# Optimization experiments

Hardware: AMD Instinct MI355X
Metric: run time of the kernel (lower is better)

The kernel has to match this reference:

```python
import jax, jax.numpy as jnp
import numpy as np

H = 128
M = 50000
L = 400000
EPS = 1e-9


def setup_inputs() -> dict:
    key = jax.random.key(0)
    ks = jax.random.split(key, 24)
    d = {
        'x_emb': jax.random.normal(ks[0], (M, H), jnp.float32),
        'child_h': jax.random.normal(ks[1], (M, H), jnp.float32),
        'child_c': jax.random.normal(ks[2], (M, H), jnp.float32),
        'pair_cand_idx': jax.random.randint(ks[3], (L,), 0, M, jnp.int32),
        'pair_child_idx': jax.random.randint(ks[4], (L,), 0, M, jnp.int32),
    }
    s = 1.0 / np.sqrt(H)
    names = ['Wi_w', 'Ui_w', 'Wf_w', 'Uf_w', 'Wo_w', 'Uo_w', 'Wc_w', 'Uc_w', 'Wa_w', 'Ua_w']
    for i, n in enumerate(names):
        d[n] = jax.random.uniform(ks[5 + i], (H, H), jnp.float32, -s, s)
    for i, n in enumerate(['Wi_b', 'Wf_b', 'Wo_b', 'Wc_b', 'Wa_b']):
        d[n] = jax.random.uniform(ks[15 + i], (H,), jnp.float32, -s, s)
    d['v_w'] = jax.random.uniform(ks[20], (H,), jnp.float32, -s, s)
    return d


def reference(x_emb, child_h, child_c, pair_cand_idx, pair_child_idx,
              Wi_w, Ui_w, Wf_w, Uf_w, Wo_w, Uo_w, Wc_w, Uc_w, Wa_w, Ua_w,
              Wi_b, Wf_b, Wo_b, Wc_b, Wa_b, v_w):
    m = x_emb.shape[0]
    ci, chi = pair_cand_idx, pair_child_idx

    # --- segment attention (torch version runs under no_grad) ---
    Ah = child_h @ Wa_w.T + Wa_b          # [M,H]
    Bx = x_emb @ Ua_w.T                   # [M,H]
    e = jnp.tanh(Ah[chi] + Bx[ci]) @ v_w  # [L]
    seg_max = jax.ops.segment_max(e, ci, num_segments=m)
    x_exp = jnp.exp(e - seg_max[ci])
    seg_sum = jax.ops.segment_sum(x_exp, ci, num_segments=m) + EPS
    attn = x_exp / seg_sum[ci]            # [L]
    h_hat = jax.ops.segment_sum(attn[:, None] * child_h[chi], ci, num_segments=m)  # [M,H]

    # --- tree-LSTM gates ---
    i_j = jax.nn.sigmoid(x_emb @ Wi_w.T + Wi_b + h_hat @ Ui_w.T)
    Wfx = x_emb @ Wf_w.T + Wf_b
    Ufh = child_h @ Uf_w.T
    f_pair = jax.nn.sigmoid(Wfx[ci] + Ufh[chi])                       # [L,H]
    sum_f_c = jax.ops.segment_sum(f_pair * child_c[chi], ci, num_segments=m)
    c_t = jnp.tanh(x_emb @ Wc_w.T + Wc_b + h_hat @ Uc_w.T)
    c = i_j * c_t + sum_f_c
    o_j = jax.nn.sigmoid(x_emb @ Wo_w.T + Wo_b + h_hat @ Uo_w.T)
    h = o_j * jnp.tanh(c)
    return (h, c)
```

## Files before the change

### kernel.cpp

```cpp
#include <hip/hip_runtime.h>
#include <cstdint>
#include <cstddef>

#define H 128
#define PSTRIDE 512

typedef __bf16 v8bf __attribute__((ext_vector_type(8)));
typedef __bf16 v4bf __attribute__((ext_vector_type(4)));
typedef float  v4f  __attribute__((ext_vector_type(4)));

__device__ __forceinline__ float ftanh(float x) {
    return 1.f - 2.f / (1.f + __expf(2.f * x));
}
__device__ __forceinline__ float fsigm(float x) {
    return 1.f / (1.f + __expf(-x));
}

__device__ __forceinline__ float red32(float s) {
    int x;
    x = __builtin_amdgcn_update_dpp(0, __float_as_int(s), 0xB1, 0xF, 0xF, true);
    s += __int_as_float(x);
    x = __builtin_amdgcn_update_dpp(0, __float_as_int(s), 0x4E, 0xF, 0xF, true);
    s += __int_as_float(x);
    x = __builtin_amdgcn_update_dpp(0, __float_as_int(s), 0x141, 0xF, 0xF, true);
    s += __int_as_float(x);
    x = __builtin_amdgcn_update_dpp(0, __float_as_int(s), 0x140, 0xF, 0xF, true);
    s += __int_as_float(x);
    x = __builtin_amdgcn_ds_swizzle(__float_as_int(s), 0x401F);
    return s + __int_as_float(x);
}

struct MatDesc {
    const __bf16* A;
    int           lda;
    const __bf16* Wb;
    const float*  bias;
    __bf16*       C;
    int           ldc;
};
struct MatBatch { MatDesc m[5]; };
struct WPtrs { const float* w[10]; };

__global__ __launch_bounds__(256) void prep_k(WPtrs wp, __bf16* __restrict__ Wb,
                                              const float* __restrict__ x,
                                              __bf16* __restrict__ xe,
                                              const int* __restrict__ ci,
                                              int* __restrict__ counts,
                                              int MH4, int L) {
    int tid = blockIdx.x * 256 + threadIdx.x;
    if (tid < 40960) {
        int mat = tid >> 12;
        int off = (tid & 4095) << 2;
        v4f a = *(const v4f*)(wp.w[mat] + off);
        v4bf b;
#pragma unroll
        for (int k = 0; k < 4; ++k) b[k] = (__bf16)a[k];
        *(v4bf*)(Wb + mat * 16384 + off) = b;
        return;
    }
    int i = tid - 40960;
    if (i < MH4) {
        v4f a = ((const v4f*)x)[i];
        v4bf ab;
#pragma unroll
        for (int k = 0; k < 4; ++k) ab[k] = (__bf16)a[k];
        ((v4bf*)xe)[i] = ab;
        return;
    }
    int l = i - MH4;
    if (l < L) atomicAdd(&counts[ci[l]], 1);
}

__global__ __launch_bounds__(256) void pair_k(const float* __restrict__ chh,
                                              const float* __restrict__ chc,
                                              const __bf16* __restrict__ Wa,
                                              const __bf16* __restrict__ Uf,
                                              const float* __restrict__ bia,
                                              __bf16* __restrict__ P,
                                              int M, int ntile) {
    const int blk = blockIdx.x;
    const int w16 = blk % 16;
    const int t   = (blk / 16) * 8 + (w16 & 7);
    const int nh  = w16 >> 3;
    if (t >= ntile) return;

    __shared__ __bf16 lds[2][64][136];

    for (int tt = threadIdx.x; tt < 2048; tt += 256) {
        int ws = tt >> 10;
        int ln = (tt >> 4) & 63;
        int k  = (tt & 15) << 3;
        const __bf16* src = ws ? Uf : Wa;
        *(v8bf*)&lds[ws][ln][k] = *(const v8bf*)(src + (nh * 64 + ln) * H + k);
    }
    __syncthreads();

    const int wave = threadIdx.x >> 6;
    const int lane = threadIdx.x & 63;
    const int quad = lane >> 4;
    const int l16  = lane & 15;
    const int r0   = t * 128 + wave * 32;

    int ra = r0 + l16;      if (ra > M - 1) ra = M - 1;
    int rb = r0 + 16 + l16; if (rb > M - 1) rb = M - 1;

    const float* p0 = chh + (size_t)ra * H + quad * 8;
    const float* p1 = chh + (size_t)rb * H + quad * 8;
    v8bf a0[4], a1[4];
#pragma unroll
    for (int k0 = 0; k0 < 4; ++k0) {
        v4f x0a = *(const v4f*)(p0 + k0 * 32);
        v4f x0b = *(const v4f*)(p0 + k0 * 32 + 4);
        v4f x1a = *(const v4f*)(p1 + k0 * 32);
        v4f x1b = *(const v4f*)(p1 + k0 * 32 + 4);
        v8bf t0, t1;
#pragma unroll
        for (int k = 0; k < 4; ++k) {
            t0[k] = (__bf16)x0a[k]; t0[k + 4] = (__bf16)x0b[k];
            t1[k] = (__bf16)x1a[k]; t1[k + 4] = (__bf16)x1b[k];
        }
        a0[k0] = t0; a1[k0] = t1;
    }

    v4f acc[2][4][2];
#pragma unroll
    for (int ws = 0; ws < 2; ++ws)
#pragma unroll
        for (int ntl = 0; ntl < 4; ++ntl)
#pragma unroll
            for (int rg = 0; rg < 2; ++rg) acc[ws][ntl][rg] = (v4f){0.f, 0.f, 0.f, 0.f};

#pragma unroll
    for (int k0 = 0; k0 < 4; ++k0) {
#pragma unroll
        for (int ntl = 0; ntl < 4; ++ntl) {
            v8bf bwa = *(const v8bf*)(&lds[0][ntl * 16 + l16][k0 * 32 + quad * 8]);
            v8bf buf = *(const v8bf*)(&lds[1][ntl * 16 + l16][k0 * 32 + quad * 8]);
            acc[0][ntl][0] = __builtin_amdgcn_mfma_f32_16x16x32_bf16(a0[k0], bwa, acc[0][ntl][0], 0, 0, 0);
            acc[0][ntl][1] = __builtin_amdgcn_mfma_f32_16x16x32_bf16(a1[k0], bwa, acc[0][ntl][1], 0, 0, 0);
            acc[1][ntl][0] = __builtin_amdgcn_mfma_f32_16x16x32_bf16(a0[k0], buf, acc[1][ntl][0], 0, 0, 0);
            acc[1][ntl][1] = __builtin_amdgcn_mfma_f32_16x16x32_bf16(a1[k0], buf, acc[1][ntl][1], 0, 0, 0);
        }
    }
    __syncthreads();

    __bf16 (*stg)[128][68] = reinterpret_cast<__bf16 (*)[128][68]>(&lds[0][0][0]);
#pragma unroll
    for (int ws = 0; ws < 2; ++ws)
#pragma unroll
        for (int ntl = 0; ntl < 4; ++ntl) {
            int lcol = ntl * 16 + l16;
            float bv = (ws == 0) ? bia[nh * 64 + lcol] : 0.f;
#pragma unroll
            for (int rg = 0; rg < 2; ++rg)
#pragma unroll
                for (int r = 0; r < 4; ++r) {
                    int lrow = wave * 32 + rg * 16 + quad * 4 + r;
                    stg[ws][lrow][lcol] = (__bf16)(acc[ws][ntl][rg][r] + bv);
                }
        }
    __syncthreads();

    for (int id = threadIdx.x; id < 2048; id += 256) {
        int lrow = id >> 4;
        int lq   = id & 15;
        int m = t * 128 + lrow;
        if (m >= M) continue;
        int q = nh * 16 + lq;
        v4f hv = *(const v4f*)(chh + (size_t)m * H + q * 4);
        v4f cv = *(const v4f*)(chc + (size_t)m * H + q * 4);
        v8bf o0, o1;
#pragma unroll
        for (int kk = 0; kk < 4; ++kk) {
            o0[kk]     = (__bf16)hv[kk];
            o0[4 + kk] = (__bf16)cv[kk];
            o1[kk]     = stg[1][lrow][lq * 4 + kk];
            o1[4 + kk] = stg[0][lrow][lq * 4 + kk];
        }
        __bf16* dst = P + (size_t)m * PSTRIDE + ((size_t)q << 4);
        *(v8bf*)dst = o0;
        *(v8bf*)(dst + 8) = o1;
    }
}

__global__ __launch_bounds__(256) void gemm_batch(MatBatch batch, int M, int ntile) {
    const int blk = blockIdx.x;
    const int g = blk / 40;
    const int w = blk % 40;
    const int j = w >> 3;
    const int t = (g << 3) | (w & 7);
    if (t >= ntile) return;
    const MatDesc d = batch.m[j];
    __shared__ __bf16 wlds[H][H + 8];

    for (int tt = threadIdx.x; tt < 2048; tt += 256) {
        int n = tt >> 4;
        int k = (tt & 15) << 3;
        *(v8bf*)&wlds[n][k] = *(const v8bf*)(d.Wb + n * H + k);
    }
    __syncthreads();

    const int wave = threadIdx.x >> 6;
    const int lane = threadIdx.x & 63;
    const int quad = lane >> 4;
    const int l16  = lane & 15;
    const int r0   = t * 128 + wave * 32;

    int ra = r0 + l16;      if (ra > M - 1) ra = M - 1;
    int rb = r0 + 16 + l16; if (rb > M - 1) rb = M - 1;

    const __bf16* p0 = d.A + (size_t)ra * d.lda + quad * 8;
    const __bf16* p1 = d.A + (size_t)rb * d.lda + quad * 8;
    v8bf a0[4], a1[4];
#pragma unroll
    for (int k0 = 0; k0 < 4; ++k0) {
        a0[k0] = *(const v8bf*)(p0 + k0 * 32);
        a1[k0] = *(const v8bf*)(p1 + k0 * 32);
    }

    v4f acc0[8], acc1[8];
#pragma unroll
    for (int nt = 0; nt < 8; ++nt) {
        acc0[nt] = (v4f){0.f, 0.f, 0.f, 0.f};
        acc1[nt] = (v4f){0.f, 0.f, 0.f, 0.f};
    }

#pragma unroll
    for (int k0 = 0; k0 < 4; ++k0) {
#pragma unroll
        for (int nt = 0; nt < 8; ++nt) {
            v8bf b = *(const v8bf*)(&wlds[nt * 16 + l16][k0 * 32 + quad * 8]);
            acc0[nt] = __builtin_amdgcn_mfma_f32_16x16x32_bf16(a0[k0], b, acc0[nt], 0, 0, 0);
            acc1[nt] = __builtin_amdgcn_mfma_f32_16x16x32_bf16(a1[k0], b, acc1[nt], 0, 0, 0);
        }
    }

#pragma unroll
    for (int nt = 0; nt < 8; ++nt) {
        int n = nt * 16 + l16;
        float bia = d.bias ? d.bias[n] : 0.f;
#pragma unroll
        for (int r = 0; r < 4; ++r) {
            int m0 = r0 + quad * 4 + r;
            int m1 = m0 + 16;
            if (m0 < M) d.C[(size_t)m0 * d.ldc + n] = (__bf16)(acc0[nt][r] + bia);
            if (m1 < M) d.C[(size_t)m1 * d.ldc + n] = (__bf16)(acc1[nt][r] + bia);
        }
    }
}

__global__ __launch_bounds__(1024) void scan_local(const int* __restrict__ counts,
                                                   int* __restrict__ excl,
                                                   int* __restrict__ bsums, int M) {
    __shared__ int s[1024];
    int tid = threadIdx.x;
    int idx = blockIdx.x * 1024 + tid;
    int v = (idx < M) ? counts[idx] : 0;
    s[tid] = v;
    __syncthreads();
    for (int off = 1; off < 1024; off <<= 1) {
        int t = (tid >= off) ? s[tid - off] : 0;
        __syncthreads();
        s[tid] += t;
        __syncthreads();
    }
    if (idx < M) excl[idx] = s[tid] - v;
    if (tid == 1023) bsums[blockIdx.x] = s[1023];
}

__global__ __launch_bounds__(1024) void scan_fused(int* __restrict__ rowptr,
                                                   int* __restrict__ cursor,
                                                   const int* __restrict__ bsums,
                                                   const int* __restrict__ counts,
                                                   int M, int nb) {
    __shared__ int s[1024];
    int t = threadIdx.x, b = blockIdx.x;
    int v = (t < nb) ? bsums[t] : 0;
    s[t] = v;
    __syncthreads();
    for (int off = 1; off < 1024; off <<= 1) {
        int tt = (t >= off) ? s[t - off] : 0;
        __syncthreads();
        s[t] += tt;
        __syncthreads();
    }
    int boff = (b == 0) ? 0 : s[b - 1];
    int idx = b * 1024 + t;
    if (idx < M) {
        int val = rowptr[idx] + boff;
        rowptr[idx] = val;
        cursor[idx] = val;
        if (idx == M - 1) rowptr[M] = val + counts[M - 1];
    }
}

__global__ __launch_bounds__(256) void scatter_k(const int* __restrict__ ci,
                                                 const int* __restrict__ chi,
                                                 int* __restrict__ cursor,
                                                 int* __restrict__ payload, int L) {
    int l = blockIdx.x * 256 + threadIdx.x;
    if (l < L) {
        int pos = atomicAdd(&cursor[ci[l]], 1);
        payload[pos] = chi[l];
    }
}

__global__ __launch_bounds__(128) void segment_fused(const int* __restrict__ rowptr,
                                                     const int* __restrict__ payload,
                                                     const float* __restrict__ vw,
                                                     const __bf16* __restrict__ Bx,
                                                     const __bf16* __restrict__ Wfx,
                                                     const __bf16* __restrict__ P,
                                                     __bf16* __restrict__ hhat,
                                                     float* __restrict__ sumfc, int M) {
    const int wl   = threadIdx.x & 63;
    const int half = wl & 32;
    const int l32  = wl & 31;
    const int m = blockIdx.x * 4 + (threadIdx.x >> 5);
    if (m >= M) return;
    const int start = rowptr[m];
    const int deg   = rowptr[m + 1] - start;
    const int h   = l32 << 2;
    const int q16 = l32 << 4;

    v4bf bx4 = *(const v4bf*)(Bx + (m << 7) + h);
    v4bf wf4 = *(const v4bf*)(Wfx + (m << 7) + h);
    v4f  vv  = *(const v4f*)(vw + h);
    float bxf[4], wff[4];
#pragma unroll
    for (int k = 0; k < 4; ++k) { bxf[k] = (float)bx4[k]; wff[k] = (float)wf4[k]; }

    int pl0 = (l32 < deg) ? payload[start + l32] : 0;
    int pl1 = (32 + l32 < deg) ? payload[start + 32 + l32] : 0;

    float denom = 0.f;
    float acch[4] = {0.f, 0.f, 0.f, 0.f};
    float accf[4] = {0.f, 0.f, 0.f, 0.f};

    const int jcap = deg < 64 ? deg : 64;
    if (jcap > 0) {
        int cj0 = __shfl(pl0, half, 64);
        const __bf16* pb0 = P + ((size_t)cj0 << 9) + q16;
        v8bf x0 = *(const v8bf*)pb0;
        v8bf x1 = *(const v8bf*)(pb0 + 8);
        for (int j = 0; j < jcap; ++j) {
            v8bf y0 = x0, y1 = x1;
            int jn = j + 1;
            if (jn < jcap) {
                int cjn = __shfl((jn & 32) ? pl1 : pl0, half | (jn & 31), 64);
                const __bf16* pbn = P + ((size_t)cjn << 9) + q16;
                x0 = *(const v8bf*)pbn;
                x1 = *(const v8bf*)(pbn + 8);
            }
            float s = 0.f;
#pragma unroll
            for (int k = 0; k < 4; ++k) s += ftanh((float)y1[4 + k] + bxf[k]) * vv[k];
            s = red32(s);
            float ex = __expf(s);
            denom += ex;
#pragma unroll
            for (int k = 0; k < 4; ++k) {
                acch[k] = fmaf(ex, (float)y0[k], acch[k]);
                accf[k] += fsigm(wff[k] + (float)y1[k]) * (float)y0[4 + k];
            }
        }
    }
    for (int j = 64; j < deg; ++j) {
        int cj = payload[start + j];
        const __bf16* pb = P + ((size_t)cj << 9) + q16;
        v8bf x0 = *(const v8bf*)pb;
        v8bf x1 = *(const v8bf*)(pb + 8);
        float s = 0.f;
#pragma unroll
        for (int k = 0; k < 4; ++k) s += ftanh((float)x1[4 + k] + bxf[k]) * vv[k];
        s = red32(s);
        float ex = __expf(s);
        denom += ex;
#pragma unroll
        for (int k = 0; k < 4; ++k) {
            acch[k] = fmaf(ex, (float)x0[k], acch[k]);
            accf[k] += fsigm(wff[k] + (float)x1[k]) * (float)x0[4 + k];
        }
    }

    float inv = 1.f / (denom + 1e-9f);
    v4bf hb;
    v4f sf;
#pragma unroll
    for (int k = 0; k < 4; ++k) { hb[k] = (__bf16)(acch[k] * inv); sf[k] = accf[k]; }
    *(v4bf*)(hhat + (size_t)m * H + h) = hb;
    *(v4f*)(sumfc + (size_t)m * H + h) = sf;
}

__global__ __launch_bounds__(256) void gemm_final(const __bf16* __restrict__ hhat,
                                                  const __bf16* __restrict__ Ui,
                                                  const __bf16* __restrict__ Uc,
                                                  const __bf16* __restrict__ Uo,
                                                  const __bf16* __restrict__ Xi,
                                                  const __bf16* __restrict__ Xc,
                                                  const __bf16* __restrict__ Xo,
                                                  const float* __restrict__ sumfc,
                                                  float* __restrict__ out, int M, int MH) {
    const int wave = threadIdx.x >> 6;
    const int lane = threadIdx.x & 63;
    const int quad = lane >> 4;
    const int l16  = lane & 15;
    const int r0   = blockIdx.x * 128 + wave * 32;
    const int nt0  = blockIdx.y * 2;

    const __bf16* p0 = hhat + (size_t)(r0 + l16) * H + quad * 8;
    const __bf16* p1 = hhat + (size_t)(r0 + 16 + l16) * H + quad * 8;
    v8bf a0[4], a1[4];
#pragma unroll
    for (int k0 = 0; k0 < 4; ++k0) {
        a0[k0] = *(const v8bf*)(p0 + k0 * 32);
        a1[k0] = *(const v8bf*)(p1 + k0 * 32);
    }

#pragma unroll
    for (int ntl = 0; ntl < 2; ++ntl) {
        const int nt = nt0 + ntl;
        const int boff = (nt * 16 + l16) * H + quad * 8;
        v4f ai0 = (v4f){0.f, 0.f, 0.f, 0.f}, ai1 = ai0;
        v4f ac0 = ai0, ac1 = ai0, ao0 = ai0, ao1 = ai0;
#pragma unroll
        for (int k0 = 0; k0 < 4; ++k0) {
            v8bf bi = *(const v8bf*)(Ui + boff + k0 * 32);
            v8bf bc = *(const v8bf*)(Uc + boff + k0 * 32);
            v8bf bo = *(const v8bf*)(Uo + boff + k0 * 32);
            ai0 = __builtin_amdgcn_mfma_f32_16x16x32_bf16(a0[k0], bi, ai0, 0, 0, 0);
            ai1 = __builtin_amdgcn_mfma_f32_16x16x32_bf16(a1[k0], bi, ai1, 0, 0, 0);
            ac0 = __builtin_amdgcn_mfma_f32_16x16x32_bf16(a0[k0], bc, ac0, 0, 0, 0);
            ac1 = __builtin_amdgcn_mfma_f32_16x16x32_bf16(a1[k0], bc, ac1, 0, 0, 0);
            ao0 = __builtin_amdgcn_mfma_f32_16x16x32_bf16(a0[k0], bo, ao0, 0, 0, 0);
            ao1 = __builtin_amdgcn_mfma_f32_16x16x32_bf16(a1[k0], bo, ao1, 0, 0, 0);
        }
        int n = nt * 16 + l16;
#pragma unroll
        for (int r = 0; r < 4; ++r) {
            int m0 = r0 + quad * 4 + r;
            if (m0 < M) {
                size_t idx = (size_t)m0 * H + n;
                float ig = fsigm((float)Xi[idx] + ai0[r]);
                float ct = ftanh((float)Xc[idx] + ac0[r]);
                float og = fsigm((float)Xo[idx] + ao0[r]);
                float c = ig * ct + sumfc[idx];
                out[idx] = og * ftanh(c);
                out[MH + idx] = c;
            }
            int m1 = m0 + 16;
            if (m1 < M) {
                size_t idx = (size_t)m1 * H + n;
                float ig = fsigm((float)Xi[idx] + ai1[r]);
                float ct = ftanh((float)Xc[idx] + ac1[r]);
                float og = fsigm((float)Xo[idx] + ao1[r]);
                float c = ig * ct + sumfc[idx];
                out[idx] = og * ftanh(c);
                out[MH + idx] = c;
            }
        }
    }
}

extern "C" void kernel_launch(void* const* d_in, const int* in_sizes, int n_in,
                              void* d_out, int out_size, void* d_ws, size_t ws_size,
                              hipStream_t stream) {
    const float* x_emb   = (const float*)d_in[0];
    const float* child_h = (const float*)d_in[1];
    const float* child_c = (const float*)d_in[2];
    const int*   ci      = (const int*)d_in[3];
    const int*   chi     = (const int*)d_in[4];
    const float* Wi_b = (const float*)d_in[15];
    const float* Wf_b = (const float*)d_in[16];
    const float* Wo_b = (const float*)d_in[17];
    const float* Wc_b = (const float*)d_in[18];
    const float* Wa_b = (const float*)d_in[19];
    const float* vw   = (const float*)d_in[20];

    const int M    = in_sizes[0] / H;
    const int L    = in_sizes[3];
    const int Mpad = (M + 127) & ~127;
    const int MH   = M * H;
    const int MH4  = MH / 4;

    char* p = (char*)d_ws;
    auto alloc = [&](size_t bytes) {
        char* r = p;
        p += (bytes + 255) & ~(size_t)255;
        return (void*)r;
    };
    size_t bfbytes = (size_t)Mpad * H * sizeof(__bf16);
    __bf16* xe16   = (__bf16*)alloc(bfbytes);
    __bf16* P      = (__bf16*)alloc((size_t)Mpad * PSTRIDE * sizeof(__bf16));
    __bf16* hhat16 = (__bf16*)alloc(bfbytes);
    __bf16* Bx16   = (__bf16*)alloc(bfbytes);
    __bf16* Wfx16  = (__bf16*)alloc(bfbytes);
    __bf16* Xi16   = (__bf16*)alloc(bfbytes);
    __bf16* Xc16   = (__bf16*)alloc(bfbytes);
    __bf16* Xo16   = (__bf16*)alloc(bfbytes);
    __bf16* Wb     = (__bf16*)alloc(10 * 16384 * sizeof(__bf16));
    float* sumfc   = (float*)alloc((size_t)MH * 4);
    int*   payload = (int*)alloc((size_t)L * 4);
    int*   counts  = (int*)alloc((size_t)M * 4);
    int*   rowptr  = (int*)alloc((size_t)(M + 1) * 4);
    int*   cursor  = (int*)alloc((size_t)M * 4);
    int*   bsums   = (int*)alloc(1024 * 4);

    hipMemsetAsync(counts, 0, (size_t)M * 4, stream);

    WPtrs wp;
    for (int k = 0; k < 10; ++k) wp.w[k] = (const float*)d_in[5 + k];
    int prep_items = 40960 + MH4 + L;
    prep_k<<<(prep_items + 255) / 256, 256, 0, stream>>>(wp, Wb, x_emb, xe16,
                                                         ci, counts, MH4, L);

    const __bf16* Wi = Wb + 0 * 16384;
    const __bf16* Ui = Wb + 1 * 16384;
    const __bf16* Wf = Wb + 2 * 16384;
    const __bf16* Uf = Wb + 3 * 16384;
    const __bf16* Wo = Wb + 4 * 16384;
    const __bf16* Uo = Wb + 5 * 16384;
    const __bf16* Wc = Wb + 6 * 16384;
    const __bf16* Uc = Wb + 7 * 16384;
    const __bf16* Wa = Wb + 8 * 16384;
    const __bf16* Ua = Wb + 9 * 16384;

    const int ntile = Mpad / 128;
    const int ntile8 = (ntile + 7) & ~7;

    pair_k<<<2 * ntile8, 256, 0, stream>>>(child_h, child_c, Wa, Uf, Wa_b, P, M, ntile);

    MatBatch ba{};
    ba.m[0] = MatDesc{xe16, H, Ua, nullptr, Bx16,  H};
    ba.m[1] = MatDesc{xe16, H, Wf, Wf_b,    Wfx16, H};
    ba.m[2] = MatDesc{xe16, H, Wi, Wi_b,    Xi16,  H};
    ba.m[3] = MatDesc{xe16, H, Wc, Wc_b,    Xc16,  H};
    ba.m[4] = MatDesc{xe16, H, Wo, Wo_b,    Xo16,  H};
    gemm_batch<<<5 * ntile8, 256, 0, stream>>>(ba, M, ntile);

    int nb = (M + 1023) / 1024;
    scan_local<<<nb, 1024, 0, stream>>>(counts, rowptr, bsums, M);
    scan_fused<<<nb, 1024, 0, stream>>>(rowptr, cursor, bsums, counts, M, nb);

    scatter_k<<<(L + 255) / 256, 256, 0, stream>>>(ci, chi, cursor, payload, L);

    segment_fused<<<(M + 3) / 4, 128, 0, stream>>>(rowptr, payload, vw, Bx16, Wfx16, P,
                                                   hhat16, sumfc, M);

    gemm_final<<<dim3(Mpad / 128, 4), 256, 0, stream>>>(hhat16, Ui, Uc, Uo, Xi16, Xc16, Xo16,
                                                        sumfc, (float*)d_out, M, MH);
}
```

Baseline: 416.1 us.

## Merge pair and batch GEMM kernels, convert weights to bf16 on load

Folds the child_h pair GEMM kernel and the five x_emb GEMMs into one launch of 7 block-groups per tile. The separate weight-conversion pass and its workspace buffer are dropped, and fp32 weights are now converted to bf16 when staged into LDS or loaded in gemm_final. This removes a kernel launch and a global round trip for the bf16 weights. In exchange every block, and every gemm_final iteration, repeats the fp32 conversion. The segment loop's software prefetch of the next P row is also removed, which may expose gather latency.

```diff
diff --git a/kernel.cpp b/kernel.cpp
--- a/kernel.cpp
+++ b/kernel.cpp
@@ -14,6 +14,15 @@
 }
 __device__ __forceinline__ float fsigm(float x) {
     return 1.f / (1.f + __expf(-x));
+}
+
+__device__ __forceinline__ v8bf cvt8(const float* p) {
+    v4f a = *(const v4f*)p;
+    v4f b = *(const v4f*)(p + 4);
+    v8bf r;
+#pragma unroll
+    for (int k = 0; k < 4; ++k) { r[k] = (__bf16)a[k]; r[4 + k] = (__bf16)b[k]; }
+    return r;
 }
 
 __device__ __forceinline__ float red32(float s) {
@@ -30,35 +39,24 @@
     return s + __int_as_float(x);
 }
 
-struct MatDesc {
-    const __bf16* A;
-    int           lda;
-    const __bf16* Wb;
-    const float*  bias;
-    __bf16*       C;
-    int           ldc;
+struct XMat { const float* W; const float* bias; __bf16* C; };
+struct GemmAll {
+    const __bf16* xe;
+    XMat xm[5];
+    const float* chh;
+    const float* chc;
+    const float* Wa;
+    const float* Uf;
+    const float* bia;
+    __bf16* P;
 };
-struct MatBatch { MatDesc m[5]; };
-struct WPtrs { const float* w[10]; };
-
-__global__ __launch_bounds__(256) void prep_k(WPtrs wp, __bf16* __restrict__ Wb,
-                                              const float* __restrict__ x,
+
+__global__ __launch_bounds__(256) void prep_k(const float* __restrict__ x,
                                               __bf16* __restrict__ xe,
                                               const int* __restrict__ ci,
                                               int* __restrict__ counts,
                                               int MH4, int L) {
-    int tid = blockIdx.x * 256 + threadIdx.x;
-    if (tid < 40960) {
-        int mat = tid >> 12;
-        int off = (tid & 4095) << 2;
-        v4f a = *(const v4f*)(wp.w[mat] + off);
-        v4bf b;
-#pragma unroll
-        for (int k = 0; k < 4; ++k) b[k] = (__bf16)a[k];
-        *(v4bf*)(Wb + mat * 16384 + off) = b;
-        return;
-    }
-    int i = tid - 40960;
+    int i = blockIdx.x * 256 + threadIdx.x;
     if (i < MH4) {
         v4f a = ((const v4f*)x)[i];
         v4bf ab;
@@ -71,29 +69,15 @@
     if (l < L) atomicAdd(&counts[ci[l]], 1);
 }
 
-__global__ __launch_bounds__(256) void pair_k(const float* __restrict__ chh,
-                                              const float* __restrict__ chc,
-                                              const __bf16* __restrict__ Wa,
-                                              const __bf16* __restrict__ Uf,
-                                              const float* __restrict__ bia,
-                                              __bf16* __restrict__ P,
-                                              int M, int ntile) {
+__global__ __launch_bounds__(256) void gemm_all(GemmAll ga, int M, int ntile) {
     const int blk = blockIdx.x;
-    const int w16 = blk % 16;
-    const int t   = (blk / 16) * 8 + (w16 & 7);
-    const int nh  = w16 >> 3;
+    const int g = blk / 56;
+    const int w = blk % 56;
+    const int j = w >> 3;
+    const int t = (g << 3) | (w & 7);
     if (t >= ntile) return;
 
-    __shared__ __bf16 lds[2][64][136];
-
-    for (int tt = threadIdx.x; tt < 2048; tt += 256) {
-        int ws = tt >> 10;
-        int ln = (tt >> 4) & 63;
-        int k  = (tt & 15) << 3;
-        const __bf16* src = ws ? Uf : Wa;
-        *(v8bf*)&lds[ws][ln][k] = *(const v8bf*)(src + (nh * 64 + ln) * H + k);
-    }
-    __syncthreads();
+    __shared__ __bf16 lds_raw[17408];
 
     const int wave = threadIdx.x >> 6;
     const int lane = threadIdx.x & 63;
@@ -104,147 +88,135 @@
     int ra = r0 + l16;      if (ra > M - 1) ra = M - 1;
     int rb = r0 + 16 + l16; if (rb > M - 1) rb = M - 1;
 
-    const float* p0 = chh + (size_t)ra * H + quad * 8;
-    const float* p1 = chh + (size_t)rb * H + quad * 8;
-    v8bf a0[4], a1[4];
-#pragma unroll
-    for (int k0 = 0; k0 < 4; ++k0) {
-        v4f x0a = *(const v4f*)(p0 + k0 * 32);
-        v4f x0b = *(const v4f*)(p0 + k0 * 32 + 4);
-        v4f x1a = *(const v4f*)(p1 + k0 * 32);
-        v4f x1b = *(const v4f*)(p1 + k0 * 32 + 4);
-        v8bf t0, t1;
-#pragma unroll
-        for (int k = 0; k < 4; ++k) {
-            t0[k] = (__bf16)x0a[k]; t0[k + 4] = (__bf16)x0b[k];
-            t1[k] = (__bf16)x1a[k]; t1[k + 4] = (__bf16)x1b[k];
-        }
-        a0[k0] = t0; a1[k0] = t1;
-    }
-
-    v4f acc[2][4][2];
-#pragma unroll
-    for (int ws = 0; ws < 2; ++ws)
-#pragma unroll
-        for (int ntl = 0; ntl < 4; ++ntl)
-#pragma unroll
-            for (int rg = 0; rg < 2; ++rg) acc[ws][ntl][rg] = (v4f){0.f, 0.f, 0.f, 0.f};
-
-#pragma unroll
-    for (int k0 = 0; k0 < 4; ++k0) {
-#pragma unroll
-        for (int ntl = 0; ntl < 4; ++ntl) {
-            v8bf bwa = *(const v8bf*)(&lds[0][ntl * 16 + l16][k0 * 32 + quad * 8]);
-            v8bf buf = *(const v8bf*)(&lds[1][ntl * 16 + l16][k0 * 32 + quad * 8]);
-            acc[0][ntl][0] = __builtin_amdgcn_mfma_f32_16x16x32_bf16(a0[k0], bwa, acc[0][ntl][0], 0, 0, 0);
-            acc[0][ntl][1] = __builtin_amdgcn_mfma_f32_16x16x32_bf16(a1[k0], bwa, acc[0][ntl][1], 0, 0, 0);
-            acc[1][ntl][0] = __builtin_amdgcn_mfma_f32_16x16x32_bf16(a0[k0], buf, acc[1][ntl][0], 0, 0, 0);
-            acc[1][ntl][1] = __builtin_amdgcn_mfma_f32_16x16x32_bf16(a1[k0], buf, acc[1][ntl][1], 0, 0, 0);
-        }
-    }
-    __syncthreads();
-
-    __bf16 (*stg)[128][68] = reinterpret_cast<__bf16 (*)[128][68]>(&lds[0][0][0]);
-#pragma unroll
-    for (int ws = 0; ws < 2; ++ws)
-#pragma unroll
-        for (int ntl = 0; ntl < 4; ++ntl) {
-            int lcol = ntl * 16 + l16;
-            float bv = (ws == 0) ? bia[nh * 64 + lcol] : 0.f;
-#pragma unroll
-            for (int rg = 0; rg < 2; ++rg)
-#pragma unroll
-                for (int r = 0; r < 4; ++r) {
-                    int lrow = wave * 32 + rg * 16 + quad * 4 + r;
-                    stg[ws][lrow][lcol] = (__bf16)(acc[ws][ntl][rg][r] + bv);
-                }
-        }
-    __syncthreads();
-
-    for (int id = threadIdx.x; id < 2048; id += 256) {
-        int lrow = id >> 4;
-        int lq   = id & 15;
-        int m = t * 128 + lrow;
-        if (m >= M) continue;
-        int q = nh * 16 + lq;
-        v4f hv = *(const v4f*)(chh + (size_t)m * H + q * 4);
-        v4f cv = *(const v4f*)(chc + (size_t)m * H + q * 4);
-        v8bf o0, o1;
-#pragma unroll
-        for (int kk = 0; kk < 4; ++kk) {
-            o0[kk]     = (__bf16)hv[kk];
-            o0[4 + kk] = (__bf16)cv[kk];
-            o1[kk]     = stg[1][lrow][lq * 4 + kk];
-            o1[4 + kk] = stg[0][lrow][lq * 4 + kk];
-        }
-        __bf16* dst = P + (size_t)m * PSTRIDE + ((size_t)q << 4);
-        *(v8bf*)dst = o0;
-        *(v8bf*)(dst + 8) = o1;
-    }
-}
-
-__global__ __launch_bounds__(256) void gemm_batch(MatBatch batch, int M, int ntile) {
-    const int blk = blockIdx.x;
-    const int g = blk / 40;
-    const int w = blk % 40;
-    const int j = w >> 3;
-    const int t = (g << 3) | (w & 7);
-    if (t >= ntile) return;
-    const MatDesc d = batch.m[j];
-    __shared__ __bf16 wlds[H][H + 8];
-
-    for (int tt = threadIdx.x; tt < 2048; tt += 256) {
-        int n = tt >> 4;
-        int k = (tt & 15) << 3;
-        *(v8bf*)&wlds[n][k] = *(const v8bf*)(d.Wb + n * H + k);
-    }
-    __syncthreads();
-
-    const int wave = threadIdx.x >> 6;
-    const int lane = threadIdx.x & 63;
-    const int quad = lane >> 4;
-    const int l16  = lane & 15;
-    const int r0   = t * 128 + wave * 32;
-
-    int ra = r0 + l16;      if (ra > M - 1) ra = M - 1;
-    int rb = r0 + 16 + l16; if (rb > M - 1) rb = M - 1;
-
-    const __bf16* p0 = d.A + (size_t)ra * d.lda + quad * 8;
-    const __bf16* p1 = d.A + (size_t)rb * d.lda + quad * 8;
-    v8bf a0[4], a1[4];
-#pragma unroll
-    for (int k0 = 0; k0 < 4; ++k0) {
-        a0[k0] = *(const v8bf*)(p0 + k0 * 32);
-        a1[k0] = *(const v8bf*)(p1 + k0 * 32);
-    }
-
-    v4f acc0[8], acc1[8];
-#pragma unroll
-    for (int nt = 0; nt < 8; ++nt) {
-        acc0[nt] = (v4f){0.f, 0.f, 0.f, 0.f};
-        acc1[nt] = (v4f){0.f, 0.f, 0.f, 0.f};
-    }
-
-#pragma unroll
-    for (int k0 = 0; k0 < 4; ++k0) {
+    if (j < 5) {
+        __bf16 (*wlds)[H + 8] = reinterpret_cast<__bf16 (*)[H + 8]>(lds_raw);
+        const float* Wf = ga.xm[j].W;
+        for (int tt = threadIdx.x; tt < 2048; tt += 256) {
+            int n = tt >> 4;
+            int k = (tt & 15) << 3;
+            *(v8bf*)&wlds[n][k] = cvt8(Wf + n * H + k);
+        }
+        __syncthreads();
+
+        const __bf16* p0 = ga.xe + (size_t)ra * H + quad * 8;
+        const __bf16* p1 = ga.xe + (size_t)rb * H + quad * 8;
+        v8bf a0[4], a1[4];
+#pragma unroll
+        for (int k0 = 0; k0 < 4; ++k0) {
+            a0[k0] = *(const v8bf*)(p0 + k0 * 32);
+            a1[k0] = *(const v8bf*)(p1 + k0 * 32);
+        }
+
+        v4f acc0[8], acc1[8];
 #pragma unroll
         for (int nt = 0; nt < 8; ++nt) {
-            v8bf b = *(const v8bf*)(&wlds[nt * 16 + l16][k0 * 32 + quad * 8]);
-            acc0[nt] = __builtin_amdgcn_mfma_f32_16x16x32_bf16(a0[k0], b, acc0[nt], 0, 0, 0);
-            acc1[nt] = __builtin_amdgcn_mfma_f32_16x16x32_bf16(a1[k0], b, acc1[nt], 0, 0, 0);
-        }
-    }
-
-#pragma unroll
-    for (int nt = 0; nt < 8; ++nt) {
-        int n = nt * 16 + l16;
-        float bia = d.bias ? d.bias[n] : 0.f;
-#pragma unroll
-        for (int r = 0; r < 4; ++r) {
-            int m0 = r0 + quad * 4 + r;
-            int m1 = m0 + 16;
-            if (m0 < M) d.C[(size_t)m0 * d.ldc + n] = (__bf16)(acc0[nt][r] + bia);
-            if (m1 < M) d.C[(size_t)m1 * d.ldc + n] = (__bf16)(acc1[nt][r] + bia);
+            acc0[nt] = (v4f){0.f, 0.f, 0.f, 0.f};
+            acc1[nt] = (v4f){0.f, 0.f, 0.f, 0.f};
+        }
+#pragma unroll
+        for (int k0 = 0; k0 < 4; ++k0) {
+#pragma unroll
+            for (int nt = 0; nt < 8; ++nt) {
+                v8bf b = *(const v8bf*)(&wlds[nt * 16 + l16][k0 * 32 + quad * 8]);
+                acc0[nt] = __builtin_amdgcn_mfma_f32_16x16x32_bf16(a0[k0], b, acc0[nt], 0, 0, 0);
+                acc1[nt] = __builtin_amdgcn_mfma_f32_16x16x32_bf16(a1[k0], b, acc1[nt], 0, 0, 0);
+            }
+        }
+
+        const float* bias = ga.xm[j].bias;
+        __bf16* C = ga.xm[j].C;
+#pragma unroll
+        for (int nt = 0; nt < 8; ++nt) {
+            int n = nt * 16 + l16;
+            float bv = bias ? bias[n] : 0.f;
+#pragma unroll
+            for (int r = 0; r < 4; ++r) {
+                int m0 = r0 + quad * 4 + r;
+                int m1 = m0 + 16;
+                if (m0 < M) C[(size_t)m0 * H + n] = (__bf16)(acc0[nt][r] + bv);
+                if (m1 < M) C[(size_t)m1 * H + n] = (__bf16)(acc1[nt][r] + bv);
+            }
+        }
+    } else {
+        const int nh = j - 5;
+        __bf16 (*lds)[64][136] = reinterpret_cast<__bf16 (*)[64][136]>(lds_raw);
+
+        for (int tt = threadIdx.x; tt < 2048; tt += 256) {
+            int ws = tt >> 10;
+            int ln = (tt >> 4) & 63;
+            int k  = (tt & 15) << 3;
+            const float* src = ws ? ga.Uf : ga.Wa;
+            *(v8bf*)&lds[ws][ln][k] = cvt8(src + (nh * 64 + ln) * H + k);
+        }
+        __syncthreads();
+
+        const float* p0 = ga.chh + (size_t)ra * H + quad * 8;
+        const float* p1 = ga.chh + (size_t)rb * H + quad * 8;
+        v8bf a0[4], a1[4];
+#pragma unroll
+        for (int k0 = 0; k0 < 4; ++k0) {
+            a0[k0] = cvt8(p0 + k0 * 32);
+            a1[k0] = cvt8(p1 + k0 * 32);
+        }
+
+        v4f acc[2][4][2];
+#pragma unroll
+        for (int ws = 0; ws < 2; ++ws)
+#pragma unroll
+            for (int ntl = 0; ntl < 4; ++ntl)
+#pragma unroll
+                for (int rg = 0; rg < 2; ++rg) acc[ws][ntl][rg] = (v4f){0.f, 0.f, 0.f, 0.f};
+
+#pragma unroll
+        for (int k0 = 0; k0 < 4; ++k0) {
+#pragma unroll
+            for (int ntl = 0; ntl < 4; ++ntl) {
+                v8bf bwa = *(const v8bf*)(&lds[0][ntl * 16 + l16][k0 * 32 + quad * 8]);
+                v8bf buf = *(const v8bf*)(&lds[1][ntl * 16 + l16][k0 * 32 + quad * 8]);
+                acc[0][ntl][0] = __builtin_amdgcn_mfma_f32_16x16x32_bf16(a0[k0], bwa, acc[0][ntl][0], 0, 0, 0);
+                acc[0][ntl][1] = __builtin_amdgcn_mfma_f32_16x16x32_bf16(a1[k0], bwa, acc[0][ntl][1], 0, 0, 0);
+                acc[1][ntl][0] = __builtin_amdgcn_mfma_f32_16x16x32_bf16(a0[k0], buf, acc[1][ntl][0], 0, 0, 0);
+                acc[1][ntl][1] = __builtin_amdgcn_mfma_f32_16x16x32_bf16(a1[k0], buf, acc[1][ntl][1], 0, 0, 0);
+            }
+        }
+        __syncthreads();
+
+        __bf16 (*stg)[128][68] = reinterpret_cast<__bf16 (*)[128][68]>(lds_raw);
+#pragma unroll
+        for (int ws = 0; ws < 2; ++ws)
+#pragma unroll
+            for (int ntl = 0; ntl < 4; ++ntl) {
+                int lcol = ntl * 16 + l16;
+                float bv = (ws == 0) ? ga.bia[nh * 64 + lcol] : 0.f;
+#pragma unroll
+                for (int rg = 0; rg < 2; ++rg)
+#pragma unroll
+                    for (int r = 0; r < 4; ++r) {
+                        int lrow = wave * 32 + rg * 16 + quad * 4 + r;
+                        stg[ws][lrow][lcol] = (__bf16)(acc[ws][ntl][rg][r] + bv);
+                    }
+            }
+        __syncthreads();
+
+        for (int id = threadIdx.x; id < 2048; id += 256) {
+            int lrow = id >> 4;
+            int lq   = id & 15;
+            int m = t * 128 + lrow;
+            if (m >= M) continue;
+            int q = nh * 16 + lq;
+            v4f hv = *(const v4f*)(ga.chh + (size_t)m * H + q * 4);
+            v4f cv = *(const v4f*)(ga.chc + (size_t)m * H + q * 4);
+            v8bf o0, o1;
+#pragma unroll
+            for (int kk = 0; kk < 4; ++kk) {
+                o0[kk]     = (__bf16)hv[kk];
+                o0[4 + kk] = (__bf16)cv[kk];
+                o1[kk]     = stg[1][lrow][lq * 4 + kk];
+                o1[4 + kk] = stg[0][lrow][lq * 4 + kk];
+            }
+            __bf16* dst = ga.P + (size_t)m * PSTRIDE + ((size_t)q << 4);
+            *(v8bf*)dst = o0;
+            *(v8bf*)(dst + 8) = o1;
         }
     }
 }
@@ -338,31 +310,21 @@
     float accf[4] = {0.f, 0.f, 0.f, 0.f};
 
     const int jcap = deg < 64 ? deg : 64;
-    if (jcap > 0) {
-        int cj0 = __shfl(pl0, half, 64);
-        const __bf16* pb0 = P + ((size_t)cj0 << 9) + q16;
-        v8bf x0 = *(const v8bf*)pb0;
-        v8bf x1 = *(const v8bf*)(pb0 + 8);
-        for (int j = 0; j < jcap; ++j) {
-            v8bf y0 = x0, y1 = x1;
-            int jn = j + 1;
-            if (jn < jcap) {
-                int cjn = __shfl((jn & 32) ? pl1 : pl0, half | (jn & 31), 64);
-                const __bf16* pbn = P + ((size_t)cjn << 9) + q16;
-                x0 = *(const v8bf*)pbn;
-                x1 = *(const v8bf*)(pbn + 8);
-            }
-            float s = 0.f;
-#pragma unroll
-            for (int k = 0; k < 4; ++k) s += ftanh((float)y1[4 + k] + bxf[k]) * vv[k];
-            s = red32(s);
-            float ex = __expf(s);
-            denom += ex;
-#pragma unroll
-            for (int k = 0; k < 4; ++k) {
-                acch[k] = fmaf(ex, (float)y0[k], acch[k]);
-                accf[k] += fsigm(wff[k] + (float)y1[k]) * (float)y0[4 + k];
-            }
+    for (int j = 0; j < jcap; ++j) {
+        int cj = __shfl((j & 32) ? pl1 : pl0, half | (j & 31), 64);
+        const __bf16* pb = P + ((size_t)cj << 9) + q16;
+        v8bf x0 = *(const v8bf*)pb;
+        v8bf x1 = *(const v8bf*)(pb + 8);
+        float s = 0.f;
+#pragma unroll
+        for (int k = 0; k < 4; ++k) s += ftanh((float)x1[4 + k] + bxf[k]) * vv[k];
+        s = red32(s);
+        float ex = __expf(s);
+        denom += ex;
+#pragma unroll
+        for (int k = 0; k < 4; ++k) {
+            acch[k] = fmaf(ex, (float)x0[k], acch[k]);
+            accf[k] += fsigm(wff[k] + (float)x1[k]) * (float)x0[4 + k];
         }
     }
     for (int j = 64; j < deg; ++j) {
@@ -393,9 +355,9 @@
 }
 
 __global__ __launch_bounds__(256) void gemm_final(const __bf16* __restrict__ hhat,
-                                                  const __bf16* __restrict__ Ui,
-                                                  const __bf16* __restrict__ Uc,
-                                                  const __bf16* __restrict__ Uo,
+                                                  const float* __restrict__ Ui,
+                                                  const float* __restrict__ Uc,
+                                                  const float* __restrict__ Uo,
                                                   const __bf16* __restrict__ Xi,
                                                   const __bf16* __restrict__ Xc,
                                                   const __bf16* __restrict__ Xo,
@@ -425,9 +387,9 @@
         v4f ac0 = ai0, ac1 = ai0, ao0 = ai0, ao1 = ai0;
 #pragma unroll
         for (int k0 = 0; k0 < 4; ++k0) {
-            v8bf bi = *(const v8bf*)(Ui + boff + k0 * 32);
-            v8bf bc = *(const v8bf*)(Uc + boff + k0 * 32);
-            v8bf bo = *(const v8bf*)(Uo + boff + k0 * 32);
+            v8bf bi = cvt8(Ui + boff + k0 * 32);
+            v8bf bc = cvt8(Uc + boff + k0 * 32);
+            v8bf bo = cvt8(Uo + boff + k0 * 32);
             ai0 = __builtin_amdgcn_mfma_f32_16x16x32_bf16(a0[k0], bi, ai0, 0, 0, 0);
             ai1 = __builtin_amdgcn_mfma_f32_16x16x32_bf16(a1[k0], bi, ai1, 0, 0, 0);
             ac0 = __builtin_amdgcn_mfma_f32_16x16x32_bf16(a0[k0], bc, ac0, 0, 0, 0);
@@ -470,6 +432,16 @@
     const float* child_c = (const float*)d_in[2];
     const int*   ci      = (const int*)d_in[3];
     const int*   chi     = (const int*)d_in[4];
+    const float* Wi_w = (const float*)d_in[5];
+    const float* Ui_w = (const float*)d_in[6];
+    const float* Wf_w = (const float*)d_in[7];
+    const float* Uf_w = (const float*)d_in[8];
+    const float* Wo_w = (const float*)d_in[9];
+    const float* Uo_w = (const float*)d_in[10];
+    const float* Wc_w = (const float*)d_in[11];
+    const float* Uc_w = (const float*)d_in[12];
+    const float* Wa_w = (const float*)d_in[13];
+    const float* Ua_w = (const float*)d_in[14];
     const float* Wi_b = (const float*)d_in[15];
     const float* Wf_b = (const float*)d_in[16];
     const float* Wo_b = (const float*)d_in[17];
@@ -498,7 +470,6 @@
     __bf16* Xi16   = (__bf16*)alloc(bfbytes);
     __bf16* Xc16   = (__bf16*)alloc(bfbytes);
     __bf16* Xo16   = (__bf16*)alloc(bfbytes);
-    __bf16* Wb     = (__bf16*)alloc(10 * 16384 * sizeof(__bf16));
     float* sumfc   = (float*)alloc((size_t)MH * 4);
     int*   payload = (int*)alloc((size_t)L * 4);
     int*   counts  = (int*)alloc((size_t)M * 4);
@@ -508,35 +479,26 @@
 
     hipMemsetAsync(counts, 0, (size_t)M * 4, stream);
 
-    WPtrs wp;
-    for (int k = 0; k < 10; ++k) wp.w[k] = (const float*)d_in[5 + k];
-    int prep_items = 40960 + MH4 + L;
-    prep_k<<<(prep_items + 255) / 256, 256, 0, stream>>>(wp, Wb, x_emb, xe16,
-                                                         ci, counts, MH4, L);
-
-    const __bf16* Wi = Wb + 0 * 16384;
-    const __bf16* Ui = Wb + 1 * 16384;
-    const __bf16* Wf = Wb + 2 * 16384;
-    const __bf16* Uf = Wb + 3 * 16384;
-    const __bf16* Wo = Wb + 4 * 16384;
-    const __bf16* Uo = Wb + 5 * 16384;
-    const __bf16* Wc = Wb + 6 * 16384;
-    const __bf16* Uc = Wb + 7 * 16384;
-    const __bf16* Wa = Wb + 8 * 16384;
-    const __bf16* Ua = Wb + 9 * 16384;
+    int prep_items = MH4 + L;
+    prep_k<<<(prep_items + 255) / 256, 256, 0, stream>>>(x_emb, xe16, ci, counts, MH4, L);
 
     const int ntile = Mpad / 128;
     const int ntile8 = (ntile + 7) & ~7;
 
-    pair_k<<<2 * ntile8, 256, 0, stream>>>(child_h, child_c, Wa, Uf, Wa_b, P, M, ntile);
-
-    MatBatch ba{};
-    ba.m[0] = MatDesc{xe16, H, Ua, nullptr, Bx16,  H};
-    ba.m[1] = MatDesc{xe16, H, Wf, Wf_b,    Wfx16, H};
-    ba.m[2] = MatDesc{xe16, H, Wi, Wi_b,    Xi16,  H};
-    ba.m[3] = MatDesc{xe16, H, Wc, Wc_b,    Xc16,  H};
-    ba.m[4] = MatDesc{xe16, H, Wo, Wo_b,    Xo16,  H};
-    gemm_batch<<<5 * ntile8, 256, 0, stream>>>(ba, M, ntile);
+    GemmAll ga{};
+    ga.xe = xe16;
+    ga.xm[0] = XMat{Ua_w, nullptr, Bx16};
+    ga.xm[1] = XMat{Wf_w, Wf_b,    Wfx16};
+    ga.xm[2] = XMat{Wi_w, Wi_b,    Xi16};
+    ga.xm[3] = XMat{Wc_w, Wc_b,    Xc16};
+    ga.xm[4] = XMat{Wo_w, Wo_b,    Xo16};
+    ga.chh = child_h;
+    ga.chc = child_c;
+    ga.Wa  = Wa_w;
+    ga.Uf  = Uf_w;
+    ga.bia = Wa_b;
+    ga.P   = P;
+    gemm_all<<<7 * ntile8, 256, 0, stream>>>(ga, M, ntile);
 
     int nb = (M + 1023) / 1024;
     scan_local<<<nb, 1024, 0, stream>>>(counts, rowptr, bsums, M);
@@ -547,6 +509,7 @@
     segment_fused<<<(M + 3) / 4, 128, 0, stream>>>(rowptr, payload, vw, Bx16, Wfx16, P,
                                                    hhat16, sumfc, M);
 
-    gemm_final<<<dim3(Mpad / 128, 4), 256, 0, stream>>>(hhat16, Ui, Uc, Uo, Xi16, Xc16, Xo16,
+    gemm_final<<<dim3(Mpad / 128, 4), 256, 0, stream>>>(hhat16, Ui_w, Uc_w, Uo_w,
+                                                        Xi16, Xc16, Xo16,
                                                         sumfc, (float*)d_out, M, MH);
 }
```

Result: slower. 435.1 us (+4.6%).
